# Performance work log

Measured on AMD Instinct MI355X. Metric: run time of the kernel, lower is better.

## Reference

```python
import jax, jax.numpy as jnp
import numpy as np

N_E = 1024
E_DIM = 256
BETA = 0.25
BATCH = 131072


def setup_inputs() -> dict:
    key = jax.random.key(0)
    k1, k2 = jax.random.split(key)
    z = jax.random.normal(k1, (BATCH, E_DIM), dtype=jnp.float32)
    # matches nn.Embedding init uniform_(-1/n_e, 1/n_e)
    emb_weight = jax.random.uniform(k2, (N_E, E_DIM), dtype=jnp.float32,
                                    minval=-1.0 / N_E, maxval=1.0 / N_E)
    return {"z": z, "emb_weight": emb_weight}


def reference(z, emb_weight):
    # z: [B, e_dim] (the module's unsqueeze/permute/view is an identity reshape)
    # squared L2 distances: [B, n_e]
    d = (jnp.sum(z * z, axis=1, keepdims=True)
         + jnp.sum(emb_weight * emb_weight, axis=1)
         - 2.0 * jnp.matmul(z, emb_weight.T))
    min_encoding_indices = jnp.argmin(d, axis=1)            # [B]
    min_encodings = jax.nn.one_hot(min_encoding_indices, N_E, dtype=z.dtype)  # [B, n_e]
    z_q = jnp.matmul(min_encodings, emb_weight)             # [B, e_dim]

    sg = jax.lax.stop_gradient
    loss = jnp.mean((sg(z_q) - z) ** 2) + BETA * jnp.mean((z_q - sg(z)) ** 2)

    # straight-through estimator
    z_q_ste = z + sg(z_q - z)

    e_mean = jnp.mean(min_encodings, axis=0)                # [n_e]
    perplexity = jnp.exp(-jnp.sum(e_mean * jnp.log(e_mean + 1e-10)))

    return (z_q_ste, loss, min_encoding_indices[:, None], perplexity)
```

## Files before the change

kernel.cpp:

```cpp
#include <hip/hip_runtime.h>

typedef __attribute__((ext_vector_type(8))) __bf16 bf16x8;
typedef __attribute__((ext_vector_type(4))) float f32x4;
typedef __attribute__((ext_vector_type(8))) unsigned short u16x8;

#define B_ROWS 131072
#define EDIM   256
#define N_E    1024
#define BMR    64
#define CHUNKS 32
#define CAP    16

#define OUT1 ((size_t)B_ROWS * EDIM)
#define OUT2 (OUT1 + 1)
#define OUT3 (OUT2 + B_ROWS)

#define WS_EMBT  0
#define WS_ESQ   524288
#define WS_COUNT 528384
#define WS_LOSS  532480

__device__ __forceinline__ unsigned short f2bf(float f) {
    unsigned u = __float_as_uint(f);
    return (unsigned short)((u + 0x7FFFu + ((u >> 16) & 1u)) >> 16);
}
__device__ __forceinline__ unsigned encf(float f) {
    unsigned u = __float_as_uint(f);
    return u ^ (unsigned)(((int)u >> 31) | 0x80000000);
}
__device__ __forceinline__ float decf(unsigned x) {
    return (x & 0x80000000u) ? __uint_as_float(x ^ 0x80000000u)
                             : __uint_as_float(~x);
}
__device__ __forceinline__ float med3f(float a, float b, float c) {
#if __has_builtin(__builtin_amdgcn_fmed3f)
    return __builtin_amdgcn_fmed3f(a, b, c);
#else
    return fmaxf(fminf(a, b), fminf(fmaxf(a, b), c));
#endif
}

__device__ inline float pw128_sq(const float* p) {
    float4 v0 = *(const float4*)p, v1 = *(const float4*)(p + 4);
    float r[8];
    r[0] = __fmul_rn(v0.x, v0.x); r[1] = __fmul_rn(v0.y, v0.y);
    r[2] = __fmul_rn(v0.z, v0.z); r[3] = __fmul_rn(v0.w, v0.w);
    r[4] = __fmul_rn(v1.x, v1.x); r[5] = __fmul_rn(v1.y, v1.y);
    r[6] = __fmul_rn(v1.z, v1.z); r[7] = __fmul_rn(v1.w, v1.w);
    for (int i = 8; i < 128; i += 8) {
        v0 = *(const float4*)(p + i); v1 = *(const float4*)(p + i + 4);
        r[0] = __fadd_rn(r[0], __fmul_rn(v0.x, v0.x));
        r[1] = __fadd_rn(r[1], __fmul_rn(v0.y, v0.y));
        r[2] = __fadd_rn(r[2], __fmul_rn(v0.z, v0.z));
        r[3] = __fadd_rn(r[3], __fmul_rn(v0.w, v0.w));
        r[4] = __fadd_rn(r[4], __fmul_rn(v1.x, v1.x));
        r[5] = __fadd_rn(r[5], __fmul_rn(v1.y, v1.y));
        r[6] = __fadd_rn(r[6], __fmul_rn(v1.z, v1.z));
        r[7] = __fadd_rn(r[7], __fmul_rn(v1.w, v1.w));
    }
    float s01 = __fadd_rn(r[0], r[1]), s23 = __fadd_rn(r[2], r[3]);
    float s45 = __fadd_rn(r[4], r[5]), s67 = __fadd_rn(r[6], r[7]);
    return __fadd_rn(__fadd_rn(s01, s23), __fadd_rn(s45, s67));
}

__device__ inline float exact_d(const float* zp, const float* ep, float zsq, float eq) {
    const float4* z4 = (const float4*)zp;
    const float4* e4 = (const float4*)ep;
    float acc = 0.f;
#pragma unroll 8
    for (int k = 0; k < 64; ++k) {
        float4 a = z4[k], b = e4[k];
        acc = __fmaf_rn(a.x, b.x, acc);
        acc = __fmaf_rn(a.y, b.y, acc);
        acc = __fmaf_rn(a.z, b.z, acc);
        acc = __fmaf_rn(a.w, b.w, acc);
    }
    return __fsub_rn(__fadd_rn(zsq, eq), 2.0f * acc);
}

__global__ void prep_emb(const float* __restrict__ emb,
                         unsigned short* __restrict__ embT,
                         float* __restrict__ esqg)
{
    int n = blockIdx.x, t = threadIdx.x;
    const float4 v = ((const float4*)(emb + (size_t)n * EDIM))[t];
    ushort4 o = { f2bf(v.x), f2bf(v.y), f2bf(v.z), f2bf(v.w) };
    int g = t >> 1, j0 = (t & 1) * 4;
    *(ushort4*)(embT + ((size_t)g * N_E + n) * 8 + j0) = o;
    if (t < 2) {
        float h = pw128_sq(emb + (size_t)n * EDIM + 128 * t);
        float ho = __shfl_xor(h, 1);
        if (t == 0) esqg[n] = __fadd_rn(h, ho);
    }
}

#define INS(s_, code_, r_)                                                  \
    {                                                                       \
        bool lt1 = (s_) < bd1[r_];                                          \
        bool lt2 = (s_) < bd2[r_];                                          \
        bd3[r_] = med3f((s_), bd2[r_], bd3[r_]);                            \
        bd2[r_] = med3f((s_), bd1[r_], bd2[r_]);                            \
        bd1[r_] = fminf((s_), bd1[r_]);                                     \
        int low_ = cp_[r_] & 0xFFFF;                                        \
        cp_[r_] = lt1 ? ((code_) | (low_ << 16))                            \
                      : (lt2 ? (low_ | ((code_) << 16)) : cp_[r_]);         \
    }

__global__ __launch_bounds__(256, 4) void vq_main(
    const float* __restrict__ z, const float* __restrict__ emb,
    const unsigned short* __restrict__ embT, const float* __restrict__ esqg,
    float* __restrict__ out, unsigned int* __restrict__ count,
    double* __restrict__ lossSum)
{
    __shared__ float esq_s[N_E];
    __shared__ float S_s[BMR];
    __shared__ unsigned cnt[BMR];
    __shared__ unsigned short list[BMR][CAP];
    __shared__ int rowbest[BMR];
    __shared__ float zq_fb;
    __shared__ unsigned long long fb4[4];
    __shared__ double red4s[4];

    const int tid  = threadIdx.x;
    const int blk  = blockIdx.x;
    const int lane = tid & 63;
    const int w    = tid >> 6;
    const int col  = lane & 15;
    const int quad = lane >> 4;
    const int row0 = w * 16;

    const float* zb = z + (size_t)blk * BMR * EDIM;

    for (int i = tid; i < N_E; i += 256) esq_s[i] = esqg[i];
    if (tid < BMR) cnt[tid] = 0u;

    bf16x8 afr[8];
    {
        int row = row0 + col;
#pragma unroll
        for (int ks = 0; ks < 8; ++ks) {
            const float* p = zb + row * EDIM + ((ks * 4 + quad) << 3);
            float4 a0 = *(const float4*)p;
            float4 a1 = *(const float4*)(p + 4);
            u16x8 t = { f2bf(a0.x), f2bf(a0.y), f2bf(a0.z), f2bf(a0.w),
                        f2bf(a1.x), f2bf(a1.y), f2bf(a1.z), f2bf(a1.w) };
            afr[ks] = *(bf16x8*)&t;
        }
    }

    if (tid < 128) {
        int row = tid >> 1, half = tid & 1;
        const float4* p4 = (const float4*)(zb + row * EDIM + half * 128);
        float4 sv = {0.f, 0.f, 0.f, 0.f};
#pragma unroll
        for (int jj = 0; jj < 32; ++jj) {
            float4 vv = p4[jj];
            sv.x += fabsf(vv.x); sv.y += fabsf(vv.y);
            sv.z += fabsf(vv.z); sv.w += fabsf(vv.w);
        }
        float sa = (sv.x + sv.y) + (sv.z + sv.w);
        float so = __shfl_xor(sa, 1);
        if (half == 0) S_s[row] = (sa + so) * 1.001f;
    }
    __syncthreads();

    int koff[8];
#pragma unroll
    for (int ks = 0; ks < 8; ++ks)
        koff[ks] = ((((ks * 4 + quad) << 10) + col) << 3);

    float bd1[4], bd2[4], bd3[4];
    int   cp_[4];
#pragma unroll
    for (int r = 0; r < 4; ++r) {
        bd1[r] = INFINITY; bd2[r] = INFINITY; bd3[r] = INFINITY; cp_[r] = 0;
    }

    for (int c = 0; c < CHUNKS; ++c) {
        const unsigned short* cb = embT + (c << 8);
        {
            u16x8 bfr[8];
#pragma unroll
            for (int ks = 0; ks < 8; ++ks)
                bfr[ks] = *(const u16x8*)(cb + koff[ks]);
            f32x4 acc = {0.f, 0.f, 0.f, 0.f};
#pragma unroll
            for (int ks = 0; ks < 8; ++ks)
                acc = __builtin_amdgcn_mfma_f32_16x16x32_bf16(afr[ks], *(bf16x8*)&bfr[ks], acc, 0, 0, 0);
            const int codeN = (c << 5) + col;
            const float eqv = esq_s[codeN];
#pragma unroll
            for (int r = 0; r < 4; ++r) {
                float s = __fmaf_rn(-2.0f, acc[r], eqv);
                INS(s, codeN, r);
            }
        }
        {
            u16x8 bfr[8];
#pragma unroll
            for (int ks = 0; ks < 8; ++ks)
                bfr[ks] = *(const u16x8*)(cb + koff[ks] + 128);
            f32x4 acc = {0.f, 0.f, 0.f, 0.f};
#pragma unroll
            for (int ks = 0; ks < 8; ++ks)
                acc = __builtin_amdgcn_mfma_f32_16x16x32_bf16(afr[ks], *(bf16x8*)&bfr[ks], acc, 0, 0, 0);
            const int codeN = (c << 5) + 16 + col;
            const float eqv = esq_s[codeN];
#pragma unroll
            for (int r = 0; r < 4; ++r) {
                float s = __fmaf_rn(-2.0f, acc[r], eqv);
                INS(s, codeN, r);
            }
        }
    }

    float th[4];
#pragma unroll
    for (int r = 0; r < 4; ++r) {
        unsigned long long kk =
            ((unsigned long long)encf(bd1[r]) << 32) | (unsigned)(cp_[r] & 0xFFFF);
#pragma unroll
        for (int msk = 1; msk <= 8; msk <<= 1) {
            unsigned long long o = __shfl_xor(kk, msk);
            if (o < kk) kk = o;
        }
        int row = row0 + quad * 4 + r;
        th[r] = decf((unsigned)(kk >> 32)) + (S_s[row] * (1.0f / 131072.0f) + 1e-4f);
    }

#pragma unroll
    for (int r = 0; r < 4; ++r) {
        int row = row0 + quad * 4 + r;
        if (__builtin_expect(bd1[r] <= th[r], 0)) {
            unsigned i = atomicAdd(&cnt[row], 1u);
            if (i < CAP) list[row][i] = (unsigned short)(cp_[r] & 0xFFFF);
        }
        if (__builtin_expect(bd2[r] <= th[r], 0)) {
            unsigned i = atomicAdd(&cnt[row], 1u);
            if (i < CAP) list[row][i] = (unsigned short)((unsigned)cp_[r] >> 16);
        }
        if (__builtin_expect(bd3[r] <= th[r], 0))
            atomicAdd(&cnt[row], 1000u);
    }
    __syncthreads();

    {
        int row = tid >> 2, j = tid & 3;
        int cn = (int)cnt[row];
        if (cn > CAP) {
            if (j == 0) rowbest[row] = -1;
        } else if (cn == 1) {
            if (j == 0) rowbest[row] = (int)list[row][0];
        } else {
            const float* zrow = zb + row * EDIM;
            float h = (j < 2) ? pw128_sq(zrow + 128 * j) : 0.f;
            int base = lane & ~3;
            float v0 = __shfl(h, base);
            float v1 = __shfl(h, base + 1);
            float zq = __fadd_rn(v0, v1);
            unsigned long long bkey = ~0ull;
            for (int i = j; i < cn; i += 4) {
                int n = (int)list[row][i];
                float d = exact_d(zrow, emb + (size_t)n * EDIM, zq, esq_s[n]);
                unsigned long long k2 = ((unsigned long long)encf(d) << 32) | (unsigned)n;
                if (k2 < bkey) bkey = k2;
            }
#pragma unroll
            for (int m = 1; m <= 2; m <<= 1) {
                unsigned long long o = __shfl_xor(bkey, m);
                if (o < bkey) bkey = o;
            }
            if (j == 0) rowbest[row] = (int)(bkey & 0xFFFFFFFFu);
        }
    }
    __syncthreads();

    for (int r = 0; r < BMR; ++r) {
        if (rowbest[r] != -1) continue;
        const float* zr = zb + r * EDIM;
        if (tid == 0)
            zq_fb = __fadd_rn(pw128_sq(zr), pw128_sq(zr + 128));
        __syncthreads();
        float zqr = zq_fb;
        unsigned long long k = ~0ull;
        for (int ci = 0; ci < 4; ++ci) {
            int n = tid + ci * 256;
            float d = exact_d(zr, emb + (size_t)n * EDIM, zqr, esq_s[n]);
            unsigned long long k2 = ((unsigned long long)encf(d) << 32) | (unsigned)n;
            if (k2 < k) k = k2;
        }
#pragma unroll
        for (int msk = 1; msk <= 32; msk <<= 1) {
            unsigned long long o = __shfl_xor(k, msk);
            if (o < k) k = o;
        }
        if (lane == 0) fb4[w] = k;
        __syncthreads();
        if (tid == 0) rowbest[r] = (int)((fb4[0] < fb4[1] ? fb4[0] : fb4[1]) <
                                         (fb4[2] < fb4[3] ? fb4[2] : fb4[3])
                                         ? (fb4[0] < fb4[1] ? fb4[0] : fb4[1])
                                         : (fb4[2] < fb4[3] ? fb4[2] : fb4[3]));
        __syncthreads();
    }

    {
        const int row = tid >> 2, q = tid & 3;
        const size_t grow = (size_t)blk * BMR + row;
        const int bn = rowbest[row];
        const float4* zp4 = (const float4*)(zb + row * EDIM);
        const float4* ebr = (const float4*)(emb + (size_t)bn * EDIM);
        float4* outr = (float4*)(out + grow * EDIM);
        double lacc = 0.0;
#pragma unroll
        for (int i = 0; i < 16; ++i) {
            int k4 = q + i * 4;
            float4 zv = zp4[k4];
            float4 ev = ebr[k4];
            float4 o; float sd;
            sd = __fsub_rn(ev.x, zv.x); o.x = __fadd_rn(zv.x, sd); lacc += (double)__fmul_rn(sd, sd);
            sd = __fsub_rn(ev.y, zv.y); o.y = __fadd_rn(zv.y, sd); lacc += (double)__fmul_rn(sd, sd);
            sd = __fsub_rn(ev.z, zv.z); o.z = __fadd_rn(zv.z, sd); lacc += (double)__fmul_rn(sd, sd);
            sd = __fsub_rn(ev.w, zv.w); o.w = __fadd_rn(zv.w, sd); lacc += (double)__fmul_rn(sd, sd);
            outr[k4] = o;
        }
        if (q == 0) {
            out[OUT2 + grow] = (float)bn;
            atomicAdd(&count[bn], 1u);
        }
#pragma unroll
        for (int msk = 1; msk <= 32; msk <<= 1) lacc += __shfl_xor(lacc, msk);
        if (lane == 0) red4s[w] = lacc;
        __syncthreads();
        if (tid == 0) atomicAdd(lossSum, red4s[0] + red4s[1] + red4s[2] + red4s[3]);
    }
}

__global__ void vq_finalize(const unsigned int* __restrict__ count,
                            const double* __restrict__ lossSum,
                            float* __restrict__ out)
{
    __shared__ double red[1024];
    int t = threadIdx.x;
    double em = (double)count[t] * (1.0 / 131072.0);
    red[t] = em * log(em + 1e-10);
    __syncthreads();
    for (int s = 512; s > 0; s >>= 1) {
        if (t < s) red[t] += red[t + s];
        __syncthreads();
    }
    if (t == 0) {
        out[OUT3] = (float)exp(-red[0]);
        double m = lossSum[0] * (1.0 / 33554432.0);
        out[OUT1] = (float)(1.25 * m);
    }
}

extern "C" void kernel_launch(void* const* d_in, const int* in_sizes, int n_in,
                              void* d_out, int out_size, void* d_ws, size_t ws_size,
                              hipStream_t stream) {
    const float* z   = (const float*)d_in[0];
    const float* emb = (const float*)d_in[1];
    float* out = (float*)d_out;

    unsigned short* embT = (unsigned short*)((char*)d_ws + WS_EMBT);
    float* esqg          = (float*)((char*)d_ws + WS_ESQ);
    unsigned int* count  = (unsigned int*)((char*)d_ws + WS_COUNT);
    double* lossSum      = (double*)((char*)d_ws + WS_LOSS);

    hipMemsetAsync((char*)d_ws + WS_COUNT, 0, 4104, stream);
    prep_emb<<<N_E, 64, 0, stream>>>(emb, embT, esqg);
    vq_main<<<B_ROWS / BMR, 256, 0, stream>>>(z, emb, embT, esqg, out, count, lossSum);
    vq_finalize<<<1, 1024, 0, stream>>>(count, lossSum, out);
}
```

Baseline: 368.5 us.

## Split VQ into scan and output kernels, double-buffer codebook fragment loads

The main kernel is split in two. A scan kernel does the bf16 MFMA distance scan and writes each row's candidate count and list into scratch space inside the output row. A second kernel, launched with 32 rows per block, re-ranks candidates exactly, handles fallback rows per wavefront without block-wide syncs, and writes z_q, indices and the loss. The scan loop now software-pipelines the B-fragment loads with two register buffers so loads overlap the MFMAs, which costs extra registers. Splitting removes the serialised fallback loop and its __syncthreads from the scan kernel, at the cost of another launch and a round trip through global memory.

New measurement: 341.3 us. -7.4%, faster.

```diff
diff --git a/kernel.cpp b/kernel.cpp
--- a/kernel.cpp
+++ b/kernel.cpp
@@ -8,8 +8,8 @@
 #define EDIM   256
 #define N_E    1024
 #define BMR    64
-#define CHUNKS 32
 #define CAP    16
+#define OROWS  32
 
 #define OUT1 ((size_t)B_ROWS * EDIM)
 #define OUT2 (OUT1 + 1)
@@ -106,20 +106,30 @@
                       : (lt2 ? (low_ | ((code_) << 16)) : cp_[r_]);         \
     }
 
-__global__ __launch_bounds__(256, 4) void vq_main(
-    const float* __restrict__ z, const float* __restrict__ emb,
-    const unsigned short* __restrict__ embT, const float* __restrict__ esqg,
-    float* __restrict__ out, unsigned int* __restrict__ count,
-    double* __restrict__ lossSum)
+#define UNIT(B_, u_)                                                        \
+    {                                                                       \
+        f32x4 acc = {0.f, 0.f, 0.f, 0.f};                                   \
+        _Pragma("unroll")                                                   \
+        for (int ks = 0; ks < 8; ++ks)                                      \
+            acc = __builtin_amdgcn_mfma_f32_16x16x32_bf16(afr[ks],          \
+                      *(bf16x8*)&B_[ks], acc, 0, 0, 0);                     \
+        const int codeN = ((u_) << 4) + col;                                \
+        const float eqv = esq_s[codeN];                                     \
+        _Pragma("unroll")                                                   \
+        for (int r = 0; r < 4; ++r) {                                       \
+            float s = __fmaf_rn(-2.0f, acc[r], eqv);                        \
+            INS(s, codeN, r);                                               \
+        }                                                                   \
+    }
+
+__global__ __launch_bounds__(256, 4) void vq_scan(
+    const float* __restrict__ z, const unsigned short* __restrict__ embT,
+    const float* __restrict__ esqg, float* __restrict__ out)
 {
     __shared__ float esq_s[N_E];
     __shared__ float S_s[BMR];
     __shared__ unsigned cnt[BMR];
     __shared__ unsigned short list[BMR][CAP];
-    __shared__ int rowbest[BMR];
-    __shared__ float zq_fb;
-    __shared__ unsigned long long fb4[4];
-    __shared__ double red4s[4];
 
     const int tid  = threadIdx.x;
     const int blk  = blockIdx.x;
@@ -164,10 +174,7 @@
     }
     __syncthreads();
 
-    int koff[8];
-#pragma unroll
-    for (int ks = 0; ks < 8; ++ks)
-        koff[ks] = ((((ks * 4 + quad) << 10) + col) << 3);
+    const unsigned short* base = embT + ((quad << 13) + (col << 3));
 
     float bd1[4], bd2[4], bd3[4];
     int   cp_[4];
@@ -176,42 +183,21 @@
         bd1[r] = INFINITY; bd2[r] = INFINITY; bd3[r] = INFINITY; cp_[r] = 0;
     }
 
-    for (int c = 0; c < CHUNKS; ++c) {
-        const unsigned short* cb = embT + (c << 8);
-        {
-            u16x8 bfr[8];
-#pragma unroll
-            for (int ks = 0; ks < 8; ++ks)
-                bfr[ks] = *(const u16x8*)(cb + koff[ks]);
-            f32x4 acc = {0.f, 0.f, 0.f, 0.f};
-#pragma unroll
-            for (int ks = 0; ks < 8; ++ks)
-                acc = __builtin_amdgcn_mfma_f32_16x16x32_bf16(afr[ks], *(bf16x8*)&bfr[ks], acc, 0, 0, 0);
-            const int codeN = (c << 5) + col;
-            const float eqv = esq_s[codeN];
-#pragma unroll
-            for (int r = 0; r < 4; ++r) {
-                float s = __fmaf_rn(-2.0f, acc[r], eqv);
-                INS(s, codeN, r);
-            }
-        }
-        {
-            u16x8 bfr[8];
-#pragma unroll
-            for (int ks = 0; ks < 8; ++ks)
-                bfr[ks] = *(const u16x8*)(cb + koff[ks] + 128);
-            f32x4 acc = {0.f, 0.f, 0.f, 0.f};
-#pragma unroll
-            for (int ks = 0; ks < 8; ++ks)
-                acc = __builtin_amdgcn_mfma_f32_16x16x32_bf16(afr[ks], *(bf16x8*)&bfr[ks], acc, 0, 0, 0);
-            const int codeN = (c << 5) + 16 + col;
-            const float eqv = esq_s[codeN];
-#pragma unroll
-            for (int r = 0; r < 4; ++r) {
-                float s = __fmaf_rn(-2.0f, acc[r], eqv);
-                INS(s, codeN, r);
-            }
-        }
+    u16x8 A[8], Bf[8];
+#pragma unroll
+    for (int ks = 0; ks < 8; ++ks) A[ks] = *(const u16x8*)(base + ks * 32768);
+
+    for (int u = 0; u < 64; u += 2) {
+        const unsigned short* pb = base + (u + 1) * 128;
+#pragma unroll
+        for (int ks = 0; ks < 8; ++ks) Bf[ks] = *(const u16x8*)(pb + ks * 32768);
+        UNIT(A, u);
+        if (u + 2 < 64) {
+            const unsigned short* pa = base + (u + 2) * 128;
+#pragma unroll
+            for (int ks = 0; ks < 8; ++ks) A[ks] = *(const u16x8*)(pa + ks * 32768);
+        }
+        UNIT(Bf, u + 1);
     }
 
     float th[4];
@@ -244,48 +230,69 @@
     }
     __syncthreads();
 
-    {
-        int row = tid >> 2, j = tid & 3;
-        int cn = (int)cnt[row];
-        if (cn > CAP) {
-            if (j == 0) rowbest[row] = -1;
-        } else if (cn == 1) {
-            if (j == 0) rowbest[row] = (int)list[row][0];
-        } else {
-            const float* zrow = zb + row * EDIM;
-            float h = (j < 2) ? pw128_sq(zrow + 128 * j) : 0.f;
-            int base = lane & ~3;
-            float v0 = __shfl(h, base);
-            float v1 = __shfl(h, base + 1);
-            float zq = __fadd_rn(v0, v1);
-            unsigned long long bkey = ~0ull;
-            for (int i = j; i < cn; i += 4) {
-                int n = (int)list[row][i];
-                float d = exact_d(zrow, emb + (size_t)n * EDIM, zq, esq_s[n]);
-                unsigned long long k2 = ((unsigned long long)encf(d) << 32) | (unsigned)n;
-                if (k2 < bkey) bkey = k2;
-            }
-#pragma unroll
-            for (int m = 1; m <= 2; m <<= 1) {
-                unsigned long long o = __shfl_xor(bkey, m);
-                if (o < bkey) bkey = o;
-            }
-            if (j == 0) rowbest[row] = (int)(bkey & 0xFFFFFFFFu);
-        }
-    }
-    __syncthreads();
-
-    for (int r = 0; r < BMR; ++r) {
-        if (rowbest[r] != -1) continue;
-        const float* zr = zb + r * EDIM;
-        if (tid == 0)
-            zq_fb = __fadd_rn(pw128_sq(zr), pw128_sq(zr + 128));
-        __syncthreads();
-        float zqr = zq_fb;
+    if (tid < BMR) {
+        int row = tid;
+        size_t grow = (size_t)blk * BMR + row;
+        unsigned* rec = (unsigned*)(out + grow * EDIM);
+        rec[0] = cnt[row];
+#pragma unroll
+        for (int k = 0; k < 8; ++k)
+            rec[1 + k] = (unsigned)list[row][2 * k]
+                       | ((unsigned)list[row][2 * k + 1] << 16);
+    }
+}
+
+__global__ void vq_output(const float* __restrict__ z, const float* __restrict__ emb,
+                          const float* __restrict__ esqg, float* __restrict__ out,
+                          unsigned int* __restrict__ count,
+                          double* __restrict__ lossSum)
+{
+    __shared__ double red4s[4];
+    const int tid  = threadIdx.x;
+    const int blk  = blockIdx.x;
+    const int lane = tid & 63;
+    const int w    = tid >> 6;
+    const int row  = tid >> 3;
+    const int q    = tid & 7;
+    const size_t grow = (size_t)blk * OROWS + row;
+    const float* zrow = z + grow * EDIM;
+    const unsigned* rec = (const unsigned*)(out + grow * EDIM);
+
+    unsigned cn = rec[0];
+    int bn = 0;
+    if (cn == 1u) {
+        bn = (int)(rec[1] & 0xFFFFu);
+    } else if (cn <= CAP) {
+        float h = (q < 2) ? pw128_sq(zrow + 128 * q) : 0.f;
+        int b8 = lane & ~7;
+        float zq = __fadd_rn(__shfl(h, b8), __shfl(h, b8 + 1));
+        unsigned long long bkey = ~0ull;
+        for (int i = q; i < (int)cn; i += 8) {
+            unsigned pr = rec[1 + (i >> 1)];
+            int n = (int)((i & 1) ? (pr >> 16) : (pr & 0xFFFFu));
+            float d = exact_d(zrow, emb + (size_t)n * EDIM, zq, esqg[n]);
+            unsigned long long k2 = ((unsigned long long)encf(d) << 32) | (unsigned)n;
+            if (k2 < bkey) bkey = k2;
+        }
+#pragma unroll
+        for (int m = 1; m <= 4; m <<= 1) {
+            unsigned long long o = __shfl_xor(bkey, m);
+            if (o < bkey) bkey = o;
+        }
+        bn = (int)(bkey & 0xFFFFFFFFu);
+    }
+    unsigned long long ball = __ballot(cn > CAP);
+    while (ball) {
+        int lb = (int)(__ffsll((long long)ball) - 1);
+        int rsel = lb >> 3;
+        size_t growo = (size_t)blk * OROWS + (w << 3) + rsel;
+        const float* zr = z + growo * EDIM;
+        float h2 = (lane < 2) ? pw128_sq(zr + 128 * lane) : 0.f;
+        float zq2 = __fadd_rn(__shfl(h2, 0), __shfl(h2, 1));
         unsigned long long k = ~0ull;
-        for (int ci = 0; ci < 4; ++ci) {
-            int n = tid + ci * 256;
-            float d = exact_d(zr, emb + (size_t)n * EDIM, zqr, esq_s[n]);
+        for (int n0 = 0; n0 < 16; ++n0) {
+            int n = lane * 16 + n0;
+            float d = exact_d(zr, emb + (size_t)n * EDIM, zq2, esqg[n]);
             unsigned long long k2 = ((unsigned long long)encf(d) << 32) | (unsigned)n;
             if (k2 < k) k = k2;
         }
@@ -294,45 +301,35 @@
             unsigned long long o = __shfl_xor(k, msk);
             if (o < k) k = o;
         }
-        if (lane == 0) fb4[w] = k;
-        __syncthreads();
-        if (tid == 0) rowbest[r] = (int)((fb4[0] < fb4[1] ? fb4[0] : fb4[1]) <
-                                         (fb4[2] < fb4[3] ? fb4[2] : fb4[3])
-                                         ? (fb4[0] < fb4[1] ? fb4[0] : fb4[1])
-                                         : (fb4[2] < fb4[3] ? fb4[2] : fb4[3]));
-        __syncthreads();
-    }
-
-    {
-        const int row = tid >> 2, q = tid & 3;
-        const size_t grow = (size_t)blk * BMR + row;
-        const int bn = rowbest[row];
-        const float4* zp4 = (const float4*)(zb + row * EDIM);
-        const float4* ebr = (const float4*)(emb + (size_t)bn * EDIM);
-        float4* outr = (float4*)(out + grow * EDIM);
-        double lacc = 0.0;
-#pragma unroll
-        for (int i = 0; i < 16; ++i) {
-            int k4 = q + i * 4;
-            float4 zv = zp4[k4];
-            float4 ev = ebr[k4];
-            float4 o; float sd;
-            sd = __fsub_rn(ev.x, zv.x); o.x = __fadd_rn(zv.x, sd); lacc += (double)__fmul_rn(sd, sd);
-            sd = __fsub_rn(ev.y, zv.y); o.y = __fadd_rn(zv.y, sd); lacc += (double)__fmul_rn(sd, sd);
-            sd = __fsub_rn(ev.z, zv.z); o.z = __fadd_rn(zv.z, sd); lacc += (double)__fmul_rn(sd, sd);
-            sd = __fsub_rn(ev.w, zv.w); o.w = __fadd_rn(zv.w, sd); lacc += (double)__fmul_rn(sd, sd);
-            outr[k4] = o;
-        }
-        if (q == 0) {
-            out[OUT2 + grow] = (float)bn;
-            atomicAdd(&count[bn], 1u);
-        }
-#pragma unroll
-        for (int msk = 1; msk <= 32; msk <<= 1) lacc += __shfl_xor(lacc, msk);
-        if (lane == 0) red4s[w] = lacc;
-        __syncthreads();
-        if (tid == 0) atomicAdd(lossSum, red4s[0] + red4s[1] + red4s[2] + red4s[3]);
-    }
+        if ((lane >> 3) == rsel) bn = (int)(k & 0xFFFFFFFFu);
+        ball &= ~(0xFFull << (lb & ~7));
+    }
+
+    const float4* zp4 = (const float4*)zrow;
+    const float4* ebr = (const float4*)(emb + (size_t)bn * EDIM);
+    float4* outr = (float4*)(out + grow * EDIM);
+    double lacc = 0.0;
+#pragma unroll
+    for (int i = 0; i < 8; ++i) {
+        int k4 = q + i * 8;
+        float4 zv = zp4[k4];
+        float4 ev = ebr[k4];
+        float4 o; float sd;
+        sd = __fsub_rn(ev.x, zv.x); o.x = __fadd_rn(zv.x, sd); lacc += (double)__fmul_rn(sd, sd);
+        sd = __fsub_rn(ev.y, zv.y); o.y = __fadd_rn(zv.y, sd); lacc += (double)__fmul_rn(sd, sd);
+        sd = __fsub_rn(ev.z, zv.z); o.z = __fadd_rn(zv.z, sd); lacc += (double)__fmul_rn(sd, sd);
+        sd = __fsub_rn(ev.w, zv.w); o.w = __fadd_rn(zv.w, sd); lacc += (double)__fmul_rn(sd, sd);
+        outr[k4] = o;
+    }
+    if (q == 0) {
+        out[OUT2 + grow] = (float)bn;
+        atomicAdd(&count[bn], 1u);
+    }
+#pragma unroll
+    for (int msk = 1; msk <= 32; msk <<= 1) lacc += __shfl_xor(lacc, msk);
+    if (lane == 0) red4s[w] = lacc;
+    __syncthreads();
+    if (tid == 0) atomicAdd(lossSum, red4s[0] + red4s[1] + red4s[2] + red4s[3]);
 }
 
 __global__ void vq_finalize(const unsigned int* __restrict__ count,
@@ -369,6 +366,7 @@
 
     hipMemsetAsync((char*)d_ws + WS_COUNT, 0, 4104, stream);
     prep_emb<<<N_E, 64, 0, stream>>>(emb, embT, esqg);
-    vq_main<<<B_ROWS / BMR, 256, 0, stream>>>(z, emb, embT, esqg, out, count, lossSum);
+    vq_scan<<<B_ROWS / BMR, 256, 0, stream>>>(z, embT, esqg, out);
+    vq_output<<<B_ROWS / OROWS, 256, 0, stream>>>(z, emb, esqg, out, count, lossSum);
     vq_finalize<<<1, 1024, 0, stream>>>(count, lossSum, out);
 }
```
